# Kernel tuning notes

Hardware: AMD Instinct MI355X
Metric: run time of the kernel (lower is better)

The kernel has to match this reference:

```python
import jax, jax.numpy as jnp
import numpy as np

INV_SQRT2 = 0.7071067811865476  # pywt haar: cA=(x0+x1)/sqrt2, cD=(x0-x1)/sqrt2


def haar_dwt2(x):
    # x: (..., H, W) with even H, W. Matches pywt.dwt2 (cA, (cH, cV, cD))
    # keys: cH='da' (detail along rows), cV='ad', cD='dd'.
    aw = (x[..., ::2] + x[..., 1::2]) * INV_SQRT2   # low-pass along W
    dw = (x[..., ::2] - x[..., 1::2]) * INV_SQRT2   # high-pass along W
    LL = (aw[..., ::2, :] + aw[..., 1::2, :]) * INV_SQRT2
    LH = (aw[..., ::2, :] - aw[..., 1::2, :]) * INV_SQRT2  # cH
    HL = (dw[..., ::2, :] + dw[..., 1::2, :]) * INV_SQRT2  # cV
    HH = (dw[..., ::2, :] - dw[..., 1::2, :]) * INV_SQRT2  # cD
    return LL, LH, HL, HH


def _interleave_h(e, o):
    out_shape = e.shape[:-2] + (2 * e.shape[-2], e.shape[-1])
    return jnp.stack([e, o], axis=-2).reshape(out_shape)


def _interleave_w(e, o):
    out_shape = e.shape[:-1] + (2 * e.shape[-1],)
    return jnp.stack([e, o], axis=-1).reshape(out_shape)


def haar_idwt2(LL, LH, HL, HH):
    # exact inverse of haar_dwt2 (== pywt.idwt2 for haar, even sizes)
    aw = _interleave_h((LL + LH) * INV_SQRT2, (LL - LH) * INV_SQRT2)
    dw = _interleave_h((HL + HH) * INV_SQRT2, (HL - HH) * INV_SQRT2)
    return _interleave_w((aw + dw) * INV_SQRT2, (aw - dw) * INV_SQRT2)


def conv2d(x, w, b, stride, pad):
    y = jax.lax.conv_general_dilated(
        x, w, (stride, stride), [(pad, pad), (pad, pad)],
        dimension_numbers=('NCHW', 'OIHW', 'NCHW'))
    return y + b[None, :, None, None]


def conv_transpose2d(x, w, b, stride, pad):
    # torch ConvTranspose2d weight layout: (in, out, kH, kW)
    k = w.shape[2]
    wt = jnp.flip(jnp.transpose(w, (1, 0, 2, 3)), (2, 3))  # -> (out,in,kH,kW)
    p = k - 1 - pad
    y = jax.lax.conv_general_dilated(
        x, wt, (1, 1), [(p, p), (p, p)], lhs_dilation=(stride, stride),
        dimension_numbers=('NCHW', 'OIHW', 'NCHW'))
    return y + b[None, :, None, None]


def setup_inputs() -> dict:
    key = jax.random.key(0)
    k1, k2, k3 = jax.random.split(key, 3)
    B, C, H, W = 32, 3, 512, 512
    x = jax.random.normal(k1, (B, C, H, W), dtype=jnp.float32)
    # kaiming-style init for the small 9->9 convs
    down_w = jax.random.normal(k2, (9, 9, 3, 3), dtype=jnp.float32) * np.sqrt(2.0 / (9 * 9))
    down_b = jnp.zeros((9,), dtype=jnp.float32)
    up_w = jax.random.normal(k3, (9, 9, 4, 4), dtype=jnp.float32) * np.sqrt(2.0 / (9 * 16))
    up_b = jnp.zeros((9,), dtype=jnp.float32)
    return {"x": x, "down_w": down_w, "down_b": down_b, "up_w": up_w, "up_b": up_b}


def reference(x, down_w, down_b, up_w, up_b):
    B, C, H, W = x.shape
    # ---- encode ----
    LL1, LH1, HL1, HH1 = haar_dwt2(x)      # (B,C,H/2,W/2)
    LL2, LH2, HL2, HH2 = haar_dwt2(LL1)    # (B,C,H/4,W/4)
    level2 = jnp.stack([LL2, LH2, HL2, HH2], axis=2).reshape(B, C * 4, H // 4, W // 4)
    level1 = jnp.stack([LH1, HL1, HH1], axis=2).reshape(B, C * 3, H // 2, W // 2)
    level1_down = conv2d(level1, down_w, down_b, stride=2, pad=1)  # (B,9,H/4,W/4)
    z = jnp.concatenate([level2, level1_down], axis=1)             # (B,21,H/4,W/4)
    # ---- decode ----
    l2 = z[:, :4 * C].reshape(B, C, 4, H // 4, W // 4)
    l1 = conv_transpose2d(z[:, 4 * C:], up_w, up_b, stride=2, pad=1)
    l1 = l1.reshape(B, C, 3, H // 2, W // 2)
    LL1r = haar_idwt2(l2[:, :, 0], l2[:, :, 1], l2[:, :, 2], l2[:, :, 3])
    x_rec = haar_idwt2(LL1r, l1[:, :, 0], l1[:, :, 1], l1[:, :, 2])
    return x_rec
```

## Files before the change

### kernel.cpp

```cpp
#include <hip/hip_runtime.h>


#define BB 32

__global__ __launch_bounds__(256) void k0_rearrange(
    const float* __restrict__ dw, const float* __restrict__ uw,
    float* __restrict__ wd, float* __restrict__ wu)
{
    const int t = threadIdx.x;
    for (int i = t; i < 729; i += 256) {
        const int o   = i % 9;
        const int q   = (i / 9) % 3;
        const int a   = (i / 27) % 3;
        const int cin = i / 81;
        wd[i] = 0.5f * dw[o * 81 + cin * 9 + a * 3 + q];
    }
    for (int i = t; i < 1296; i += 256) {
        const int o = i % 9; int r = i / 9;
        const int dj = r & 1; const int di = (r >> 1) & 1; r >>= 2;
        const int ct = r & 1; const int rt = (r >> 1) & 1; const int cin = r >> 2;
        wu[i] = uw[cin * 144 + o * 16 + (3 - di - 2 * rt) * 4 + (3 - dj - 2 * ct)];
    }
}

__global__ __launch_bounds__(256) void k1_dwt_down(
    const float* __restrict__ x,
    const float* __restrict__ wd,
    const float* __restrict__ db,
    float* __restrict__ LL1,
    float* __restrict__ y)
{
    __shared__ float bnd[9 * 561];

    const int t   = threadIdx.x;
    const int bid = blockIdx.x;
    const int swz = (bid & 7) * 512 + (bid >> 3);
    const int b   = swz >> 7;
    const int tin = swz & 127;
    const int I0  = (tin >> 3) * 8;
    const int J0  = (tin & 7) * 16;

    for (int it = t; it < 1683; it += 256) {
        const int ch = it / 561;
        const int rc = it - ch * 561;
        const int lr = rc / 33;
        const int lc = rc - lr * 33;
        const int rB = 2 * I0 - 1 + lr;
        const int cB = 2 * J0 - 1 + lc;
        float x00 = 0.f, x01 = 0.f, x10 = 0.f, x11 = 0.f;
        if (rB >= 0 && cB >= 0) {
            const float* xp =
                x + (((size_t)b * 3 + ch) * 512 + 2 * rB) * 512 + 2 * cB;
            const float2 v0 = *reinterpret_cast<const float2*>(xp);
            const float2 v1 = *reinterpret_cast<const float2*>(xp + 512);
            x00 = v0.x; x01 = v0.y; x10 = v1.x; x11 = v1.y;
        }
        const float s0 = x00 + x01, d0 = x00 - x01;
        const float s1 = x10 + x11, d1 = x10 - x11;
        bnd[(ch * 3 + 0) * 561 + lr * 33 + lc] = s0 - s1;
        bnd[(ch * 3 + 1) * 561 + lr * 33 + lc] = d0 + d1;
        bnd[(ch * 3 + 2) * 561 + lr * 33 + lc] = d0 - d1;
        if (lr >= 1 && lc >= 1)
            LL1[(((size_t)b * 3 + ch) * 256 + rB) * 256 + cB] = (s0 + s1) * 0.5f;
    }
    __syncthreads();

    const int og = t >> 7;
    const int tl = t & 127;
    const int ti = tl >> 4;
    const int tj = tl & 15;
    const int I  = I0 + ti;
    const int J  = J0 + tj;

    if (og == 0) {
        float acc[5];
#pragma unroll
        for (int o = 0; o < 5; ++o) acc[o] = db[o];
        for (int cin = 0; cin < 9; ++cin) {
            float v[3][3];
#pragma unroll
            for (int a = 0; a < 3; ++a)
#pragma unroll
                for (int q = 0; q < 3; ++q)
                    v[a][q] = bnd[cin * 561 + (2 * ti + a) * 33 + 2 * tj + q];
            const float* wc = wd + cin * 81;
#pragma unroll
            for (int a = 0; a < 3; ++a)
#pragma unroll
                for (int q = 0; q < 3; ++q) {
                    const float vv = v[a][q];
                    const float* w9 = wc + (a * 3 + q) * 9;
#pragma unroll
                    for (int o = 0; o < 5; ++o) acc[o] += vv * w9[o];
                }
        }
#pragma unroll
        for (int o = 0; o < 5; ++o)
            y[(((size_t)b * 9 + o) * 128 + I) * 128 + J] = acc[o];
    } else {
        float acc[4];
#pragma unroll
        for (int o = 0; o < 4; ++o) acc[o] = db[5 + o];
        for (int cin = 0; cin < 9; ++cin) {
            float v[3][3];
#pragma unroll
            for (int a = 0; a < 3; ++a)
#pragma unroll
                for (int q = 0; q < 3; ++q)
                    v[a][q] = bnd[cin * 561 + (2 * ti + a) * 33 + 2 * tj + q];
            const float* wc = wd + cin * 81;
#pragma unroll
            for (int a = 0; a < 3; ++a)
#pragma unroll
                for (int q = 0; q < 3; ++q) {
                    const float vv = v[a][q];
                    const float* w9 = wc + (a * 3 + q) * 9 + 5;
#pragma unroll
                    for (int o = 0; o < 4; ++o) acc[o] += vv * w9[o];
                }
        }
#pragma unroll
        for (int o = 0; o < 4; ++o)
            y[(((size_t)b * 9 + 5 + o) * 128 + I) * 128 + J] = acc[o];
    }
}

__global__ __launch_bounds__(256, 4) void k2_up_idwt(
    const float* __restrict__ yg,
    const float* __restrict__ wu,
    const float* __restrict__ ub,
    const float* __restrict__ LL1,
    float* __restrict__ out)
{
    __shared__ float ysh[9][18][19];

    const int t    = threadIdx.x;
    const int b    = blockIdx.x >> 6;
    const int tile = blockIdx.x & 63;
    const int r0   = (tile >> 3) << 5;
    const int c0   = (tile & 7) << 5;
    const int p0   = (r0 >> 1) - 1;
    const int q0   = (c0 >> 1) - 1;

    for (int item = t; item < 9 * 324; item += 256) {
        const int cin = item / 324;
        int rem       = item - cin * 324;
        const int lp  = rem / 18;
        const int lq  = rem - lp * 18;
        const int p   = p0 + lp, q = q0 + lq;
        float v = 0.f;
        if (p >= 0 && p < 128 && q >= 0 && q < 128)
            v = yg[(((size_t)b * 9 + cin) * 128 + p) * 128 + q];
        ysh[cin][lp][lq] = v;
    }
    __syncthreads();

    const int i2 = t >> 4;
    const int j2 = t & 15;

    float acc[2][2][9];
#pragma unroll
    for (int di = 0; di < 2; ++di)
#pragma unroll
        for (int dj = 0; dj < 2; ++dj)
#pragma unroll
            for (int o = 0; o < 9; ++o) acc[di][dj][o] = ub[o];

    for (int cin = 0; cin < 9; ++cin) {
        float yv[3][3];
#pragma unroll
        for (int r = 0; r < 3; ++r)
#pragma unroll
            for (int c = 0; c < 3; ++c)
                yv[r][c] = ysh[cin][i2 + r][j2 + c];
        const float* wc = wu + cin * 144;
#pragma unroll
        for (int rt = 0; rt < 2; ++rt)
#pragma unroll
            for (int ct = 0; ct < 2; ++ct) {
                const float* wg = wc + (rt * 2 + ct) * 36;
#pragma unroll
                for (int di = 0; di < 2; ++di)
#pragma unroll
                    for (int dj = 0; dj < 2; ++dj) {
                        const float vv = yv[di + rt][dj + ct];
                        const float* w9 = wg + (di * 2 + dj) * 9;
#pragma unroll
                        for (int o = 0; o < 9; ++o)
                            acc[di][dj][o] += vv * w9[o];
                    }
            }
    }

#pragma unroll
    for (int cc = 0; cc < 3; ++cc) {
#pragma unroll
        for (int di = 0; di < 2; ++di) {
            const int I = r0 + 2 * i2 + di;
            const int J = c0 + 2 * j2;
            const float2 llv = *reinterpret_cast<const float2*>(
                LL1 + (((size_t)b * 3 + cc) * 256 + I) * 256 + J);
            float4 top, bot;
            {
                const float ll = llv.x;
                const float lh = acc[di][0][cc * 3 + 0];
                const float hl = acc[di][0][cc * 3 + 1];
                const float hh = acc[di][0][cc * 3 + 2];
                const float e0 = ll + lh, od0 = ll - lh;
                const float e1 = hl + hh, od1 = hl - hh;
                top.x = (e0 + e1) * 0.5f; top.y = (e0 - e1) * 0.5f;
                bot.x = (od0 + od1) * 0.5f; bot.y = (od0 - od1) * 0.5f;
            }
            {
                const float ll = llv.y;
                const float lh = acc[di][1][cc * 3 + 0];
                const float hl = acc[di][1][cc * 3 + 1];
                const float hh = acc[di][1][cc * 3 + 2];
                const float e0 = ll + lh, od0 = ll - lh;
                const float e1 = hl + hh, od1 = hl - hh;
                top.z = (e0 + e1) * 0.5f; top.w = (e0 - e1) * 0.5f;
                bot.z = (od0 + od1) * 0.5f; bot.w = (od0 - od1) * 0.5f;
            }
            float* op = out + (((size_t)b * 3 + cc) * 512 + 2 * I) * 512 + 2 * J;
            *reinterpret_cast<float4*>(op) = top;
            *reinterpret_cast<float4*>(op + 512) = bot;
        }
    }
}

extern "C" void kernel_launch(void* const* d_in, const int* in_sizes, int n_in,
                              void* d_out, int out_size, void* d_ws, size_t ws_size,
                              hipStream_t stream) {
    const float* x  = (const float*)d_in[0];
    const float* dw = (const float*)d_in[1];
    const float* db = (const float*)d_in[2];
    const float* uw = (const float*)d_in[3];
    const float* ub = (const float*)d_in[4];
    float* outp = (float*)d_out;

    float* wsf = (float*)d_ws;
    float* wd  = wsf;
    float* wu  = wsf + 768;
    float* LL1 = wsf + 2304;
    float* y   = LL1 + (size_t)BB * 3 * 256 * 256;

    k0_rearrange<<<dim3(1), dim3(256), 0, stream>>>(dw, uw, wd, wu);
    k1_dwt_down<<<dim3(4096), dim3(256), 0, stream>>>(x, wd, db, LL1, y);
    k2_up_idwt<<<dim3(BB * 64), dim3(256), 0, stream>>>(y, wu, ub, LL1, outp);
}
```

Baseline: 85.29 us.

## Split DWT band computation from downsampling conv into separate kernels

Splits the fused DWT+conv kernel into two. The first does coalesced float4 reads of x and writes the three detail bands (into the output buffer as scratch) plus LL1. The second conv kernel then loads the precomputed bands into shared memory. This removes the strided float2 gathers and redundant halo DWT work from the conv kernel, but adds an extra global round-trip of about 9 channels at 256x256 per batch and one more launch.

```diff
diff --git a/kernel.cpp b/kernel.cpp
--- a/kernel.cpp
+++ b/kernel.cpp
@@ -23,11 +23,49 @@
     }
 }
 
-__global__ __launch_bounds__(256) void k1_dwt_down(
+__global__ __launch_bounds__(256) void k1a_bands(
     const float* __restrict__ x,
+    float* __restrict__ bd,
+    float* __restrict__ LL1)
+{
+    const int t   = threadIdx.x;
+    const int bid = blockIdx.x;
+    const int swz = (bid & 7) * 1536 + (bid >> 3);
+    const int bc  = swz >> 7;
+    const int r2  = swz & 127;
+    const int row = 2 * r2 + (t >> 7);
+    const int s   = t & 127;
+
+    const float* xp = x + (((size_t)bc * 512 + 2 * row) * 512) + 4 * s;
+    const float4 A  = *reinterpret_cast<const float4*>(xp);
+    const float4 Bv = *reinterpret_cast<const float4*>(xp + 512);
+
+    float2 lh, hl, hh, ll;
+    {
+        const float s0 = A.x + A.y, d0 = A.x - A.y;
+        const float s1 = Bv.x + Bv.y, d1 = Bv.x - Bv.y;
+        lh.x = s0 - s1; hl.x = d0 + d1; hh.x = d0 - d1; ll.x = (s0 + s1) * 0.5f;
+    }
+    {
+        const float s0 = A.z + A.w, d0 = A.z - A.w;
+        const float s1 = Bv.z + Bv.w, d1 = Bv.z - Bv.w;
+        lh.y = s0 - s1; hl.y = d0 + d1; hh.y = d0 - d1; ll.y = (s0 + s1) * 0.5f;
+    }
+
+    const int b  = bc / 3;
+    const int ch = bc - 3 * b;
+    float* base = bd + ((((size_t)b * 9 + ch * 3) * 256 + row) * 256) + 2 * s;
+    *reinterpret_cast<float2*>(base)           = lh;
+    *reinterpret_cast<float2*>(base + 65536)   = hl;
+    *reinterpret_cast<float2*>(base + 131072)  = hh;
+    *reinterpret_cast<float2*>(
+        LL1 + (((size_t)bc * 256 + row) * 256) + 2 * s) = ll;
+}
+
+__global__ __launch_bounds__(256) void k1b_conv(
+    const float* __restrict__ bd,
     const float* __restrict__ wd,
     const float* __restrict__ db,
-    float* __restrict__ LL1,
     float* __restrict__ y)
 {
     __shared__ float bnd[9 * 561];
@@ -40,28 +78,17 @@
     const int I0  = (tin >> 3) * 8;
     const int J0  = (tin & 7) * 16;
 
-    for (int it = t; it < 1683; it += 256) {
-        const int ch = it / 561;
-        const int rc = it - ch * 561;
+    for (int it = t; it < 5049; it += 256) {
+        const int p  = it / 561;
+        const int rc = it - p * 561;
         const int lr = rc / 33;
         const int lc = rc - lr * 33;
         const int rB = 2 * I0 - 1 + lr;
         const int cB = 2 * J0 - 1 + lc;
-        float x00 = 0.f, x01 = 0.f, x10 = 0.f, x11 = 0.f;
-        if (rB >= 0 && cB >= 0) {
-            const float* xp =
-                x + (((size_t)b * 3 + ch) * 512 + 2 * rB) * 512 + 2 * cB;
-            const float2 v0 = *reinterpret_cast<const float2*>(xp);
-            const float2 v1 = *reinterpret_cast<const float2*>(xp + 512);
-            x00 = v0.x; x01 = v0.y; x10 = v1.x; x11 = v1.y;
-        }
-        const float s0 = x00 + x01, d0 = x00 - x01;
-        const float s1 = x10 + x11, d1 = x10 - x11;
-        bnd[(ch * 3 + 0) * 561 + lr * 33 + lc] = s0 - s1;
-        bnd[(ch * 3 + 1) * 561 + lr * 33 + lc] = d0 + d1;
-        bnd[(ch * 3 + 2) * 561 + lr * 33 + lc] = d0 - d1;
-        if (lr >= 1 && lc >= 1)
-            LL1[(((size_t)b * 3 + ch) * 256 + rB) * 256 + cB] = (s0 + s1) * 0.5f;
+        float v = 0.f;
+        if (rB >= 0 && cB >= 0)
+            v = bd[(((size_t)b * 9 + p) * 256 + rB) * 256 + cB];
+        bnd[p * 561 + lr * 33 + lc] = v;
     }
     __syncthreads();
 
@@ -243,8 +270,10 @@
     float* wu  = wsf + 768;
     float* LL1 = wsf + 2304;
     float* y   = LL1 + (size_t)BB * 3 * 256 * 256;
+    float* bd  = outp;
 
     k0_rearrange<<<dim3(1), dim3(256), 0, stream>>>(dw, uw, wd, wu);
-    k1_dwt_down<<<dim3(4096), dim3(256), 0, stream>>>(x, wd, db, LL1, y);
+    k1a_bands<<<dim3(12288), dim3(256), 0, stream>>>(x, bd, LL1);
+    k1b_conv<<<dim3(4096), dim3(256), 0, stream>>>(bd, wd, db, y);
     k2_up_idwt<<<dim3(BB * 64), dim3(256), 0, stream>>>(y, wu, ub, LL1, outp);
 }
```

New measurement: 114.4 us. 34.1% more time.
